# Kernel tuning notes

Hardware: AMD Instinct MI355X
Metric: run time of the kernel (lower is better)

The kernel has to match this reference:

```python
import jax, jax.numpy as jnp
import numpy as np
from jax import lax

B, N, C, NP, NS, H, L = 2, 16384, 256, 2048, 32, 4, 2
DFF = 2 * C
RADIUS = 1.0
EPS = 1e-5


def setup_inputs() -> dict:
    key = jax.random.key(0)
    ks = jax.random.split(key, 12)
    s = 0.02
    f32 = jnp.float32
    return {
        "xyz": jax.random.normal(ks[0], (B, N, 3), f32),
        "features": jax.random.normal(ks[1], (B, C, N), f32),
        # positional encoding: Conv1x1(3->C/2)+BN(eval)+ReLU, Conv1x1(C/2->C)
        "pe1_w": jax.random.normal(ks[2], (C // 2, 3), f32) * s,
        "pe1_b": jnp.zeros((C // 2,), f32),
        "bn_g": jnp.ones((C // 2,), f32),
        "bn_b": jnp.zeros((C // 2,), f32),
        "bn_m": jnp.zeros((C // 2,), f32),
        "bn_v": jnp.ones((C // 2,), f32),
        "pe2_w": jax.random.normal(ks[3], (C, C // 2), f32) * s,
        "pe2_b": jnp.zeros((C,), f32),
        # L pre-norm transformer encoder layers (stacked on leading dim)
        "ipw": jax.random.normal(ks[4], (L, 3 * C, C), f32) * s,
        "ipb": jnp.zeros((L, 3 * C), f32),
        "opw": jax.random.normal(ks[5], (L, C, C), f32) * s,
        "opb": jnp.zeros((L, C), f32),
        "ln1s": jnp.ones((L, C), f32), "ln1b": jnp.zeros((L, C), f32),
        "ln2s": jnp.ones((L, C), f32), "ln2b": jnp.zeros((L, C), f32),
        "fc1w": jax.random.normal(ks[6], (L, DFF, C), f32) * s,
        "fc1b": jnp.zeros((L, DFF), f32),
        "fc2w": jax.random.normal(ks[7], (L, C, DFF), f32) * s,
        "fc2b": jnp.zeros((L, C), f32),
    }


def _fps(xyz, npoint):
    # D-FPS starting from point 0 (pointnet2 convention). xyz: [B,N,3]
    b, n, _ = xyz.shape

    def step(carry, _):
        dists, far = carry
        centroid = jnp.take_along_axis(xyz, far[:, None, None], axis=1)  # [B,1,3]
        d = jnp.sum((xyz - centroid) ** 2, -1)
        dists = jnp.minimum(dists, d)
        return (dists, jnp.argmax(dists, -1).astype(jnp.int32)), far

    init = (jnp.full((b, n), 1e10, jnp.float32), jnp.zeros((b,), jnp.int32))
    _, idx = lax.scan(step, init, None, length=npoint)
    return idx.T  # [B, npoint]


def _ball_query(xyz, new_xyz, radius, ns):
    # first <=ns points within radius, padded with the first hit. [B,NP,NS]
    n = xyz.shape[1]
    d2 = jnp.sum((new_xyz[:, :, None, :] - xyz[:, None, :, :]) ** 2, -1)  # [B,NP,N]
    scores = jnp.where(d2 < radius * radius, jnp.arange(n, dtype=jnp.int32), n)
    svals = jnp.sort(scores, axis=-1)[..., :ns]
    order = jnp.argsort(scores, axis=-1)[..., :ns].astype(jnp.int32)
    valid = svals < n
    return jnp.where(valid, order, order[..., :1])


def _ln(x, s, b):
    m = jnp.mean(x, -1, keepdims=True)
    v = jnp.var(x, -1, keepdims=True)
    return (x - m) * lax.rsqrt(v + EPS) * s + b


def _mha(x, w, bias, ow, ob):
    # x: [S, Bn, D] (seq-first, like nn.MultiheadAttention)
    S, Bn, D = x.shape
    hd = D // H
    qkv = x @ w.T + bias
    q, k, v = jnp.split(qkv, 3, -1)
    rs = lambda t: t.reshape(S, Bn, H, hd).transpose(1, 2, 0, 3)  # [Bn,H,S,hd]
    q, k, v = rs(q), rs(k), rs(v)
    att = jax.nn.softmax(jnp.einsum('bhqd,bhkd->bhqk', q, k) * (1.0 / np.sqrt(hd)), -1)
    o = jnp.einsum('bhqk,bhkd->bhqd', att, v).transpose(2, 0, 1, 3).reshape(S, Bn, D)
    return o @ ow.T + ob


def reference(xyz, features, pe1_w, pe1_b, bn_g, bn_b, bn_m, bn_v, pe2_w, pe2_b,
              ipw, ipb, opw, opb, ln1s, ln1b, ln2s, ln2b, fc1w, fc1b, fc2w, fc2b):
    # --- sample + group ---
    fps_idx = _fps(lax.stop_gradient(xyz), NP)                       # [B,NP]
    new_xyz = jnp.take_along_axis(xyz, fps_idx[:, :, None], axis=1)  # [B,NP,3]
    idx = _ball_query(lax.stop_gradient(xyz), lax.stop_gradient(new_xyz), RADIUS, NS)
    g_xyz = jax.vmap(lambda p, i: p[i])(xyz, idx) - new_xyz[:, :, None, :]  # [B,NP,NS,3]
    g_xyz = g_xyz.transpose(0, 3, 1, 2)                              # [B,3,NP,NS]
    g_feat = jax.vmap(lambda f, i: f[:, i])(features, idx)           # [B,C,NP,NS]
    # --- positional encoding (conv1x1 + BN(eval) + ReLU, conv1x1) ---
    h = jnp.einsum('oc,bcps->bops', pe1_w, g_xyz) + pe1_b[None, :, None, None]
    h = (h - bn_m[None, :, None, None]) * lax.rsqrt(bn_v + EPS)[None, :, None, None]
    h = jax.nn.relu(h * bn_g[None, :, None, None] + bn_b[None, :, None, None])
    pe = jnp.einsum('oc,bcps->bops', pe2_w, h) + pe2_b[None, :, None, None]
    x = g_feat + pe                                                  # [B,C,NP,NS]
    # --- local transformer over each neighborhood (seq len = NS) ---
    x = x.transpose(0, 2, 1, 3).reshape(B * NP, C, NS).transpose(2, 0, 1)  # [NS,B*NP,C]
    for l in range(L):
        x = _ln(x, ln1s[l], ln1b[l])
        x = x + _mha(x, ipw[l], ipb[l], opw[l], opb[l])
        x = _ln(x, ln2s[l], ln2b[l])
        x = x + jax.nn.relu(x @ fc1w[l].T + fc1b[l]) @ fc2w[l].T + fc2b[l]
    tf = x.transpose(1, 2, 0).reshape(B, NP, C, NS).transpose(0, 2, 1, 3)  # [B,C,NP,NS]
    Lf = NP * NS

    def scat(feat_b, tf_b, idx_b):
        idx_f = idx_b.reshape(-1)          # [Lf]
        ff = tf_b.reshape(C, -1)           # [C,Lf]
        pos = jnp.arange(Lf, dtype=jnp.int32)
        first = jax.ops.segment_min(pos, idx_f, num_segments=N)  # [N], maxint if absent
        valid = first < Lf
        safe = jnp.where(valid, first, 0)
        return jnp.where(valid[None, :], ff[:, safe], feat_b)    # [C,N]

    out = jax.vmap(scat)(features, tf, idx)  # [B,C,N]
    return out.transpose(0, 2, 1)            # [B,N,C]
```

## Files before the change

kernel.cpp:

```cpp
#include <hip/hip_runtime.h>

#define NB 2
#define NN 16384
#define NC 256
#define NPp 2048
#define NSs 32
#define NH 4
#define HDh 64
#define NL 2
#define NDFF 512
#define LFv (NPp*NSs)
#define LNEPS 1e-5f
#define NBLK 256
#define NTHR 512

typedef short s16x8 __attribute__((ext_vector_type(8)));
typedef float f32x4 __attribute__((ext_vector_type(4)));
typedef float f32x2 __attribute__((ext_vector_type(2)));
typedef unsigned short u16;
typedef unsigned long long u64;

struct CtlBlock { int prog[2]; int ctr1; int ctr2; int bar; };

__device__ __forceinline__ u16 f2bf(float f){
  unsigned u = __float_as_uint(f);
  u += 0x7fffu + ((u>>16)&1u);
  return (u16)(u>>16);
}

__device__ __forceinline__ f32x4 mfma16(s16x8 a, s16x8 b, f32x4 c){
  return __builtin_amdgcn_mfma_f32_16x16x32_bf16(a, b, c, 0, 0, 0);
}

__device__ __forceinline__ f32x2 pk_add(f32x2 a, f32x2 b){
  f32x2 d; asm("v_pk_add_f32 %0, %1, %2" : "=v"(d) : "v"(a), "v"(b)); return d;
}
__device__ __forceinline__ f32x2 pk_mul(f32x2 a, f32x2 b){
  f32x2 d; asm("v_pk_mul_f32 %0, %1, %2" : "=v"(d) : "v"(a), "v"(b)); return d;
}

#define DPP_FMAX(v, ctrl) do { \
  int _iv = __float_as_int(v); \
  int _sh = __builtin_amdgcn_update_dpp(_iv, _iv, (ctrl), 0xF, 0xF, false); \
  (v) = fmaxf((v), __int_as_float(_sh)); \
} while(0)

#define DPP_IMIN(v, ctrl) do { \
  int _sh = __builtin_amdgcn_update_dpp((v), (v), (ctrl), 0xF, 0xF, false); \
  (v) = (_sh < (v)) ? _sh : (v); \
} while(0)

struct SMem {
  u64  masks[256];
  u64  keybuf[4];
  float xs[32][NC];
  u16  xn[32][264];
  u16  qb[32][776];
  u16  pb[NH][32][40];
  int  idx_sh[32];
  float gx_sh[32][3];
  float wcoord[2][8][4];
  int  misc[16];
  int  win[32];
};

__global__ void k_prep(const float* __restrict__ ipw, const float* __restrict__ opw,
                       const float* __restrict__ fc1w, const float* __restrict__ fc2w,
                       const float* __restrict__ pe2w,
                       const float* __restrict__ bng, const float* __restrict__ bnb,
                       const float* __restrict__ bnm, const float* __restrict__ bnv,
                       u16* ipwb, u16* opwb, u16* fc1wb, u16* fc2wb, u16* pe2wb,
                       float* bnsc, float* bnsh, int* first, CtlBlock* ctl){
  const int i0 = blockIdx.x*blockDim.x + threadIdx.x;
  const int stride = gridDim.x*blockDim.x;
  for (int i=i0; i<NL*768*NC; i+=stride) ipwb[i] = f2bf(ipw[i]);
  for (int i=i0; i<NL*NC*NC; i+=stride)  opwb[i] = f2bf(opw[i]);
  for (int i=i0; i<NL*NDFF*NC; i+=stride) fc1wb[i] = f2bf(fc1w[i]);
  for (int i=i0; i<NL*NC*NDFF; i+=stride) fc2wb[i] = f2bf(fc2w[i]);
  for (int i=i0; i<NC*128; i+=stride)    pe2wb[i] = f2bf(pe2w[i]);
  for (int i=i0; i<NB*NN; i+=stride)     first[i] = LFv;
  for (int i=i0; i<128; i+=stride){
    float sc = bng[i]*rsqrtf(bnv[i]+LNEPS);
    bnsc[i] = sc; bnsh[i] = bnb[i] - bnm[i]*sc;
  }
  if (i0 == 0){
    ctl->prog[0] = -1; ctl->prog[1] = -1;
    ctl->ctr1 = 0; ctl->ctr2 = 0; ctl->bar = 0;
  }
}

__global__ __launch_bounds__(256) void k_featT(const float* __restrict__ feat,
                                               float* __restrict__ featT){
  __shared__ float T[32][33];
  const int b = blockIdx.y;
  const int n0 = blockIdx.x*32;
  const int t = threadIdx.x;
  const int tn = t & 31, tc = t >> 5;
  for (int cb=0; cb<NC; cb+=32){
    #pragma unroll
    for (int i=0;i<32;i+=8)
      T[tc+i][tn] = feat[((size_t)b*NC + cb+tc+i)*NN + n0+tn];
    __syncthreads();
    #pragma unroll
    for (int i=0;i<32;i+=8)
      featT[((size_t)b*NN + n0+tc+i)*NC + cb+tn] = T[tn][tc+i];
    __syncthreads();
  }
}

__device__ void fps_run(int b, const float* __restrict__ xyz,
                        float* __restrict__ newxyz, CtlBlock* ctl, SMem& sm){
#pragma clang fp contract(off)
  const int t = threadIdx.x;
  const int lane = t & 63, wid = t >> 6;
  const float* xb = xyz + (size_t)b*NN*3;
  f32x2 px2[16], py2[16], pz2[16], dd2[16];
  #pragma unroll
  for (int m=0;m<16;m++){
    int i0 = t + (2*m)*NTHR, i1 = t + (2*m+1)*NTHR;
    px2[m] = f32x2{xb[i0*3],   xb[i1*3]};
    py2[m] = f32x2{xb[i0*3+1], xb[i1*3+1]};
    pz2[m] = f32x2{xb[i0*3+2], xb[i1*3+2]};
    dd2[m] = f32x2{1e10f, 1e10f};
  }
  if (t < 4) sm.keybuf[t] = 0ull;
  float wx = xb[0], wy = xb[1], wz = xb[2];
  if (t==0){
    newxyz[(size_t)b*NPp*3+0]=wx;
    newxyz[(size_t)b*NPp*3+1]=wy;
    newxyz[(size_t)b*NPp*3+2]=wz;
    __hip_atomic_store(&ctl->prog[b], 0, __ATOMIC_RELEASE, __HIP_MEMORY_SCOPE_AGENT);
  }
  float ncx=-wx, ncy=-wy, ncz=-wz;
  __syncthreads();
  for (int step=1; step<NPp; ++step){
    const f32x2 ncx2={ncx,ncx}, ncy2={ncy,ncy}, ncz2={ncz,ncz};
    #pragma unroll
    for (int m=0;m<16;m++){
      f32x2 dx = pk_add(px2[m], ncx2);
      f32x2 dy = pk_add(py2[m], ncy2);
      f32x2 dz = pk_add(pz2[m], ncz2);
      f32x2 s  = pk_add(pk_add(pk_mul(dx,dx), pk_mul(dy,dy)), pk_mul(dz,dz));
      f32x2 d  = dd2[m];
      d.x = fminf(d.x, s.x);
      d.y = fminf(d.y, s.y);
      dd2[m] = d;
    }
    float h8[8];
    #pragma unroll
    for (int q=0;q<8;q++)
      h8[q] = fmaxf(fmaxf(dd2[2*q].x, dd2[2*q].y), fmaxf(dd2[2*q+1].x, dd2[2*q+1].y));
    float M = fmaxf(fmaxf(fmaxf(h8[0],h8[1]),fmaxf(h8[2],h8[3])),
                    fmaxf(fmaxf(h8[4],h8[5]),fmaxf(h8[6],h8[7])));
    DPP_FMAX(M, 0x111); DPP_FMAX(M, 0x112); DPP_FMAX(M, 0x114); DPP_FMAX(M, 0x118);
    DPP_FMAX(M, 0x142); DPP_FMAX(M, 0x143);
    const unsigned Mb = (unsigned)__builtin_amdgcn_readlane(__float_as_int(M), 63);
    const float Ms = __int_as_float((int)Mb);
    int li = 0x7fffffff;
    #pragma unroll
    for (int m=15;m>=0;m--){
      if (dd2[m].y == Ms) li = t + (2*m+1)*NTHR;
      if (dd2[m].x == Ms) li = t + (2*m)*NTHR;
    }
    DPP_IMIN(li, 0x111); DPP_IMIN(li, 0x112); DPP_IMIN(li, 0x114); DPP_IMIN(li, 0x118);
    DPP_IMIN(li, 0x142); DPP_IMIN(li, 0x143);
    const int li63 = __builtin_amdgcn_readlane(li, 63);
    const int kb = step & 3, cb = step & 1;
    if (lane==0){
      u64 key = ((u64)Mb << 32) | (unsigned)(0x7fffffff - li63);
      atomicMax(&sm.keybuf[kb], key);
      const float* cp = xb + (size_t)li63*3;
      sm.wcoord[cb][wid][0]=cp[0]; sm.wcoord[cb][wid][1]=cp[1]; sm.wcoord[cb][wid][2]=cp[2];
    }
    __syncthreads();
    const u64 kk = sm.keybuf[kb];
    const int widx = 0x7fffffff - (int)(unsigned)(kk & 0xffffffffu);
    const int wv = (widx & (NTHR-1)) >> 6;
    const float nx = sm.wcoord[cb][wv][0];
    const float ny = sm.wcoord[cb][wv][1];
    const float nz = sm.wcoord[cb][wv][2];
    ncx=-nx; ncy=-ny; ncz=-nz;
    if (t==0){
      newxyz[((size_t)b*NPp+step)*3+0]=nx;
      newxyz[((size_t)b*NPp+step)*3+1]=ny;
      newxyz[((size_t)b*NPp+step)*3+2]=nz;
      sm.keybuf[(step+2)&3] = 0ull;
      if ((step & 7) == 7 || step == NPp-1)
        __hip_atomic_store(&ctl->prog[b], step, __ATOMIC_RELEASE, __HIP_MEMORY_SCOPE_AGENT);
    }
  }
}

__device__ void seq_ballq(const float* __restrict__ xb, float cx, float cy, float cz,
                          SMem& sm, int t, int lane, int wid){
#pragma clang fp contract(off)
  for (int it=0; it<32; ++it){
    int cid = wid*32 + it;
    int i = cid*64 + lane;
    float dx=xb[i*3]-cx, dy=xb[i*3+1]-cy, dz=xb[i*3+2]-cz;
    float d2=(dx*dx+dy*dy)+dz*dz;
    u64 m = __ballot(d2 < 1.0f);
    if (lane==0) sm.masks[cid] = m;
  }
  __syncthreads();
  if (wid==0){
    u64 mk[4]; int cnt=0;
    #pragma unroll
    for (int j=0;j<4;j++){ mk[j]=sm.masks[lane*4+j]; cnt += __popcll(mk[j]); }
    int inc = cnt;
    #pragma unroll
    for (int ofs=1; ofs<64; ofs<<=1){
      int v = __shfl_up(inc, ofs);
      if (lane >= ofs) inc += v;
    }
    int r = inc - cnt;
    int tot = __shfl(inc, 63);
    #pragma unroll
    for (int j=0;j<4;j++){
      u64 msk = mk[j];
      int base = (lane*4+j)*64;
      while (msk && r < NSs){
        int bpos = __ffsll(msk)-1;
        sm.idx_sh[r] = base + bpos;
        msk &= msk-1;
        ++r;
      }
      if (r >= NSs) break;
    }
    int cc = tot < NSs ? tot : NSs;
    int pv = (tot > 0) ? sm.idx_sh[0] : 0;
    if (lane < NSs && lane >= cc) sm.idx_sh[lane] = pv;
  }
  __syncthreads();
}

__device__ __forceinline__ void ln_block512(SMem& sm, const float* __restrict__ s_,
                                            const float* __restrict__ b_, int t){
  const int s = t >> 4, j = t & 15;
  float v[16];
  float sum = 0.f;
  #pragma unroll
  for (int k=0;k<16;k++){ v[k]=sm.xs[s][j*16+k]; sum += v[k]; }
  #pragma unroll
  for (int m=1;m<16;m<<=1) sum += __shfl_xor(sum, m);
  const float mean = sum * (1.f/256.f);
  float vs = 0.f;
  #pragma unroll
  for (int k=0;k<16;k++){ float d=v[k]-mean; vs += d*d; }
  #pragma unroll
  for (int m=1;m<16;m<<=1) vs += __shfl_xor(vs, m);
  const float rstd = rsqrtf(vs*(1.f/256.f) + LNEPS);
  #pragma unroll
  for (int k=0;k<16;k++){
    int c = j*16+k;
    float y = (v[k]-mean)*rstd*s_[c] + b_[c];
    sm.xs[s][c] = y;
    sm.xn[s][c] = f2bf(y);
  }
}

__device__ void seq_pe_tf(SMem& sm, int b, int p,
    const float* __restrict__ xyz, const float* __restrict__ features,
    const float* __restrict__ featT, int useT, const float* __restrict__ newxyz,
    const float* __restrict__ pe1w, const float* __restrict__ pe1b,
    const float* __restrict__ bnsc, const float* __restrict__ bnsh,
    const u16* __restrict__ pe2wb, const float* __restrict__ pe2b,
    const u16* __restrict__ ipwb, const float* __restrict__ ipb,
    const u16* __restrict__ opwb, const float* __restrict__ opb,
    const float* __restrict__ ln1s, const float* __restrict__ ln1b,
    const float* __restrict__ ln2s, const float* __restrict__ ln2b,
    const u16* __restrict__ fc1wb, const float* __restrict__ fc1b,
    const u16* __restrict__ fc2wb, const float* __restrict__ fc2b){
  const int t = threadIdx.x, lane = t & 63, wid = t >> 6;
  const int c15 = lane & 15, g4 = lane >> 4;

  if (t < 96){
    int s = t/3, d = t%3;
    sm.gx_sh[s][d] = xyz[((size_t)b*NN + sm.idx_sh[s])*3 + d] - newxyz[(size_t)p*3 + d];
  }
  if (useT){
    for (int e=t; e<32*NC; e+=NTHR){
      int s=e>>8, c=e&255;
      sm.xs[s][c] = featT[((size_t)b*NN + sm.idx_sh[s])*NC + c];
    }
  } else {
    for (int e=t; e<32*NC; e+=NTHR){
      int s=e>>8, c=e&255;
      sm.xs[s][c] = features[((size_t)b*NC + c)*NN + sm.idx_sh[s]];
    }
  }
  __syncthreads();
  for (int i=t; i<32*128; i+=NTHR){
    int s = i >> 7, o = i & 127;
    float h = pe1w[o*3]*sm.gx_sh[s][0] + pe1w[o*3+1]*sm.gx_sh[s][1] + pe1w[o*3+2]*sm.gx_sh[s][2] + pe1b[o];
    h = h*bnsc[o] + bnsh[o];
    sm.xn[s][o] = f2bf(h > 0.f ? h : 0.f);
  }
  __syncthreads();
  for (int tt=wid; tt<32; tt+=8){
    int m0 = (tt & 1)*16, n0 = (tt >> 1)*16;
    f32x4 acc = {0.f,0.f,0.f,0.f};
    #pragma unroll
    for (int kk=0; kk<4; kk++){
      s16x8 a = *(const s16x8*)&sm.xn[m0+c15][kk*32 + g4*8];
      s16x8 bb = *(const s16x8*)&pe2wb[(size_t)(n0+c15)*128 + kk*32 + g4*8];
      acc = mfma16(a, bb, acc);
    }
    int col = n0 + c15;
    float bias = pe2b[col];
    #pragma unroll
    for (int r=0;r<4;r++) sm.xs[m0 + g4*4 + r][col] += acc[r] + bias;
  }
  __syncthreads();

  for (int l=0; l<NL; ++l){
    ln_block512(sm, ln1s + l*NC, ln1b + l*NC, t);
    __syncthreads();
    const u16* Wq = ipwb + (size_t)l*768*NC;
    const float* bq = ipb + l*768;
    for (int tt=wid; tt<96; tt+=8){
      int m0 = (tt & 1)*16, n0 = (tt >> 1)*16;
      f32x4 acc = {0.f,0.f,0.f,0.f};
      #pragma unroll
      for (int kk=0;kk<8;kk++){
        s16x8 a = *(const s16x8*)&sm.xn[m0+c15][kk*32 + g4*8];
        s16x8 bb = *(const s16x8*)&Wq[(size_t)(n0+c15)*NC + kk*32 + g4*8];
        acc = mfma16(a, bb, acc);
      }
      int col = n0 + c15;
      float bias = bq[col];
      #pragma unroll
      for (int r=0;r<4;r++) sm.qb[m0 + g4*4 + r][col] = f2bf(acc[r] + bias);
    }
    __syncthreads();
    {
      const int h = wid & 3;
      const int mt = wid >> 2;
      f32x4 lac[2];
      #pragma unroll
      for (int nt=0;nt<2;nt++){
        f32x4 acc = {0.f,0.f,0.f,0.f};
        #pragma unroll
        for (int kk=0;kk<2;kk++){
          s16x8 a = *(const s16x8*)&sm.qb[mt*16+c15][h*HDh + kk*32 + g4*8];
          s16x8 bb = *(const s16x8*)&sm.qb[nt*16+c15][256 + h*HDh + kk*32 + g4*8];
          acc = mfma16(a, bb, acc);
        }
        lac[nt] = acc;
      }
      #pragma unroll
      for (int r=0;r<4;r++){
        float v0 = lac[0][r]*0.125f, v1 = lac[1][r]*0.125f;
        float mx = fmaxf(v0, v1);
        #pragma unroll
        for (int m=1;m<16;m<<=1) mx = fmaxf(mx, __shfl_xor(mx, m));
        float e0 = expf(v0-mx), e1 = expf(v1-mx);
        float smm = e0 + e1;
        #pragma unroll
        for (int m=1;m<16;m<<=1) smm += __shfl_xor(smm, m);
        float inv = 1.f/smm;
        int row = mt*16 + g4*4 + r;
        sm.pb[h][row][c15]    = f2bf(e0*inv);
        sm.pb[h][row][16+c15] = f2bf(e1*inv);
      }
      f32x4 oac[4];
      #pragma unroll
      for (int nt=0;nt<4;nt++){
        s16x8 bb;
        #pragma unroll
        for (int e=0;e<8;e++) bb[e] = (short)sm.qb[g4*8+e][512 + h*HDh + nt*16 + c15];
        f32x4 acc = {0.f,0.f,0.f,0.f};
        s16x8 a = *(const s16x8*)&sm.pb[h][mt*16+c15][g4*8];
        oac[nt] = mfma16(a, bb, acc);
      }
      __syncthreads();
      #pragma unroll
      for (int nt=0;nt<4;nt++)
        #pragma unroll
        for (int r=0;r<4;r++)
          sm.xn[mt*16 + g4*4 + r][h*HDh + nt*16 + c15] = f2bf(oac[nt][r]);
    }
    __syncthreads();
    const u16* Wo = opwb + (size_t)l*NC*NC;
    const float* bo = opb + l*NC;
    for (int tt=wid; tt<32; tt+=8){
      int m0 = (tt & 1)*16, n0 = (tt >> 1)*16;
      f32x4 acc = {0.f,0.f,0.f,0.f};
      #pragma unroll
      for (int kk=0;kk<8;kk++){
        s16x8 a = *(const s16x8*)&sm.xn[m0+c15][kk*32 + g4*8];
        s16x8 bb = *(const s16x8*)&Wo[(size_t)(n0+c15)*NC + kk*32 + g4*8];
        acc = mfma16(a, bb, acc);
      }
      int col = n0 + c15;
      float bias = bo[col];
      #pragma unroll
      for (int r=0;r<4;r++) sm.xs[m0 + g4*4 + r][col] += acc[r] + bias;
    }
    __syncthreads();
    ln_block512(sm, ln2s + l*NC, ln2b + l*NC, t);
    __syncthreads();
    const u16* W1 = fc1wb + (size_t)l*NDFF*NC;
    for (int tt=wid; tt<64; tt+=8){
      int m0 = (tt & 1)*16, n0 = (tt >> 1)*16;
      f32x4 acc = {0.f,0.f,0.f,0.f};
      #pragma unroll
      for (int kk=0;kk<8;kk++){
        s16x8 a = *(const s16x8*)&sm.xn[m0+c15][kk*32 + g4*8];
        s16x8 bb = *(const s16x8*)&W1[(size_t)(n0+c15)*NC + kk*32 + g4*8];
        acc = mfma16(a, bb, acc);
      }
      int col = n0 + c15;
      float bias = fc1b[l*NDFF + col];
      #pragma unroll
      for (int r=0;r<4;r++){
        float v = acc[r] + bias;
        sm.qb[m0 + g4*4 + r][col] = f2bf(v > 0.f ? v : 0.f);
      }
    }
    __syncthreads();
    const u16* W2 = fc2wb + (size_t)l*NC*NDFF;
    for (int tt=wid; tt<32; tt+=8){
      int m0 = (tt & 1)*16, n0 = (tt >> 1)*16;
      f32x4 acc = {0.f,0.f,0.f,0.f};
      #pragma unroll
      for (int kk=0;kk<16;kk++){
        s16x8 a = *(const s16x8*)&sm.qb[m0+c15][kk*32 + g4*8];
        s16x8 bb = *(const s16x8*)&W2[(size_t)(n0+c15)*NDFF + kk*32 + g4*8];
        acc = mfma16(a, bb, acc);
      }
      int col = n0 + c15;
      float bias = fc2b[l*NC + col];
      #pragma unroll
      for (int r=0;r<4;r++) sm.xs[m0 + g4*4 + r][col] += acc[r] + bias;
    }
    __syncthreads();
  }
}

__global__ __launch_bounds__(NTHR,1) void k_mega(
    const float* __restrict__ xyz, const float* __restrict__ features,
    const float* __restrict__ featT, int useT,
    float* __restrict__ newxyz, int* __restrict__ first, CtlBlock* ctl,
    const float* __restrict__ pe1w, const float* __restrict__ pe1b,
    const float* __restrict__ bnsc, const float* __restrict__ bnsh,
    const u16* __restrict__ pe2wb, const float* __restrict__ pe2b,
    const u16* __restrict__ ipwb, const float* __restrict__ ipb,
    const u16* __restrict__ opwb, const float* __restrict__ opb,
    const float* __restrict__ ln1s, const float* __restrict__ ln1b,
    const float* __restrict__ ln2s, const float* __restrict__ ln2b,
    const u16* __restrict__ fc1wb, const float* __restrict__ fc1b,
    const u16* __restrict__ fc2wb, const float* __restrict__ fc2b,
    float* __restrict__ out){
  __shared__ SMem sm;
  const int t = threadIdx.x, lane = t & 63, wid = t >> 6;

  if (blockIdx.x < NB){
    fps_run(blockIdx.x, xyz, newxyz, ctl, sm);
  } else {
    for (;;){
      if (t==0) sm.misc[1] = atomicAdd(&ctl->ctr1, 1);
      __syncthreads();
      int p = sm.misc[1];
      if (p >= NB*NPp) break;
      int b = p >> 11, pp = p & (NPp-1);
      if (t==0){
        while (__hip_atomic_load(&ctl->prog[b], __ATOMIC_RELAXED, __HIP_MEMORY_SCOPE_AGENT) < pp)
          __builtin_amdgcn_s_sleep(2);
        __builtin_amdgcn_fence(__ATOMIC_ACQUIRE, "agent");
      }
      __syncthreads();
      float cx = newxyz[(size_t)p*3], cy = newxyz[(size_t)p*3+1], cz = newxyz[(size_t)p*3+2];
      seq_ballq(xyz + (size_t)b*NN*3, cx, cy, cz, sm, t, lane, wid);
      if (t < NSs) atomicMin(&first[b*NN + sm.idx_sh[t]], pp*NSs + t);
      __syncthreads();
    }
  }

  __syncthreads();
  if (t==0){
    __builtin_amdgcn_fence(__ATOMIC_RELEASE, "agent");
    __hip_atomic_fetch_add(&ctl->bar, 1, __ATOMIC_RELAXED, __HIP_MEMORY_SCOPE_AGENT);
    while (__hip_atomic_load(&ctl->bar, __ATOMIC_RELAXED, __HIP_MEMORY_SCOPE_AGENT) < NBLK)
      __builtin_amdgcn_s_sleep(8);
    __builtin_amdgcn_fence(__ATOMIC_ACQUIRE, "agent");
  }
  __syncthreads();

  for (;;){
    if (t==0) sm.misc[1] = atomicAdd(&ctl->ctr2, 1);
    __syncthreads();
    int p = sm.misc[1];
    if (p >= NB*NPp) break;
    int b = p >> 11, pp = p & (NPp-1);
    float cx = newxyz[(size_t)p*3], cy = newxyz[(size_t)p*3+1], cz = newxyz[(size_t)p*3+2];
    seq_ballq(xyz + (size_t)b*NN*3, cx, cy, cz, sm, t, lane, wid);
    if (t==0) sm.misc[2] = 0;
    __syncthreads();
    if (t < NSs){
      int pos = pp*NSs + t;
      int f = __hip_atomic_load(&first[b*NN + sm.idx_sh[t]], __ATOMIC_RELAXED, __HIP_MEMORY_SCOPE_AGENT);
      int w = (f == pos) ? 1 : 0;
      sm.win[t] = w;
      if (w) atomicOr(&sm.misc[2], 1);
    }
    __syncthreads();
    if (!sm.misc[2]) continue;
    seq_pe_tf(sm, b, p, xyz, features, featT, useT, newxyz,
              pe1w, pe1b, bnsc, bnsh, pe2wb, pe2b, ipwb, ipb, opwb, opb,
              ln1s, ln1b, ln2s, ln2b, fc1wb, fc1b, fc2wb, fc2b);
    for (int e=t; e<NSs*NC; e+=NTHR){
      int s = e >> 8, c = e & 255;
      if (sm.win[s]) out[((size_t)b*NN + sm.idx_sh[s])*NC + c] = sm.xs[s][c];
    }
    __syncthreads();
  }
}

__global__ __launch_bounds__(256) void k_outfill_T(const float* __restrict__ featT,
                                                   const int* __restrict__ first,
                                                   float* __restrict__ out){
  const int t = threadIdx.x;
  for (int rr=0; rr<8; ++rr){
    int row = blockIdx.x*8 + rr;
    if (first[row] == LFv)
      out[(size_t)row*NC + t] = featT[(size_t)row*NC + t];
  }
}

__global__ __launch_bounds__(256) void k_outfill_noT(const float* __restrict__ feat,
                                                     const int* __restrict__ first,
                                                     float* __restrict__ out){
  __shared__ float T[32][33];
  const int b = blockIdx.y;
  const int n0 = blockIdx.x*32;
  const int t = threadIdx.x;
  const int tn = t & 31, tc = t >> 5;
  for (int cb=0; cb<NC; cb+=32){
    #pragma unroll
    for (int i=0;i<32;i+=8)
      T[tc+i][tn] = feat[((size_t)b*NC + cb+tc+i)*NN + n0+tn];
    __syncthreads();
    #pragma unroll
    for (int i=0;i<32;i+=8){
      int n = n0 + tc + i;
      if (first[b*NN+n] == LFv)
        out[((size_t)b*NN + n)*NC + cb+tn] = T[tn][tc+i];
    }
    __syncthreads();
  }
}

extern "C" void kernel_launch(void* const* d_in, const int* in_sizes, int n_in,
                              void* d_out, int out_size, void* d_ws, size_t ws_size,
                              hipStream_t stream){
  const float* xyz   = (const float*)d_in[0];
  const float* feat  = (const float*)d_in[1];
  const float* pe1w  = (const float*)d_in[2];
  const float* pe1b  = (const float*)d_in[3];
  const float* bng   = (const float*)d_in[4];
  const float* bnb   = (const float*)d_in[5];
  const float* bnm   = (const float*)d_in[6];
  const float* bnv   = (const float*)d_in[7];
  const float* pe2w  = (const float*)d_in[8];
  const float* pe2b  = (const float*)d_in[9];
  const float* ipw   = (const float*)d_in[10];
  const float* ipb   = (const float*)d_in[11];
  const float* opw   = (const float*)d_in[12];
  const float* opb   = (const float*)d_in[13];
  const float* ln1s  = (const float*)d_in[14];
  const float* ln1b  = (const float*)d_in[15];
  const float* ln2s  = (const float*)d_in[16];
  const float* ln2b  = (const float*)d_in[17];
  const float* fc1w  = (const float*)d_in[18];
  const float* fc1b  = (const float*)d_in[19];
  const float* fc2w  = (const float*)d_in[20];
  const float* fc2b  = (const float*)d_in[21];
  float* out = (float*)d_out;

  char* ws = (char*)d_ws;
  size_t off = 0;
  auto alloc = [&](size_t bytes)->void*{
    void* p = ws + off;
    off = (off + bytes + 255) & ~(size_t)255;
    return p;
  };
  float* newxyz  = (float*)alloc((size_t)NB*NPp*3*4);
  int*   first   = (int*)  alloc((size_t)NB*NN*4);
  CtlBlock* ctl  = (CtlBlock*)alloc(sizeof(CtlBlock));
  float* bnsc    = (float*)alloc(128*4);
  float* bnsh    = (float*)alloc(128*4);
  u16*   ipwb    = (u16*)  alloc((size_t)NL*768*NC*2);
  u16*   opwb    = (u16*)  alloc((size_t)NL*NC*NC*2);
  u16*   fc1wb   = (u16*)  alloc((size_t)NL*NDFF*NC*2);
  u16*   fc2wb   = (u16*)  alloc((size_t)NL*NC*NDFF*2);
  u16*   pe2wb   = (u16*)  alloc((size_t)NC*128*2);
  float* featT   = (float*)(ws + off);
  int useT = (off + (size_t)NB*NN*NC*4 <= ws_size) ? 1 : 0;

  k_prep<<<512, 256, 0, stream>>>(ipw, opw, fc1w, fc2w, pe2w, bng, bnb, bnm, bnv,
                                  ipwb, opwb, fc1wb, fc2wb, pe2wb, bnsc, bnsh, first, ctl);
  if (useT)
    k_featT<<<dim3(NN/32, NB), 256, 0, stream>>>(feat, featT);

  const float* featT_c = featT;
  void* kargs[] = {
    (void*)&xyz, (void*)&feat, (void*)&featT_c, (void*)&useT,
    (void*)&newxyz, (void*)&first, (void*)&ctl,
    (void*)&pe1w, (void*)&pe1b, (void*)&bnsc, (void*)&bnsh,
    (void*)&pe2wb, (void*)&pe2b, (void*)&ipwb, (void*)&ipb,
    (void*)&opwb, (void*)&opb, (void*)&ln1s, (void*)&ln1b,
    (void*)&ln2s, (void*)&ln2b, (void*)&fc1wb, (void*)&fc1b,
    (void*)&fc2wb, (void*)&fc2b, (void*)&out };
  hipLaunchCooperativeKernel((void*)k_mega, dim3(NBLK), dim3(NTHR), kargs, 0, stream);

  if (useT)
    k_outfill_T<<<(NB*NN)/8, 256, 0, stream>>>(featT, first, out);
  else
    k_outfill_noT<<<dim3(NN/32, NB), 256, 0, stream>>>(feat, first, out);
  (void)in_sizes; (void)n_in; (void)out_size;
}
```

Baseline: 4.474 ms.

## Replace FPS progress counter with per-centroid ready flags and register-held winner coords

FPS now takes the winning centroid's coordinates from registers through a slot switch, so it no longer reloads them from global memory. Centroids are batched in shared memory and published every 8 steps as packed u64 stores, each followed by a per-point ready flag. Consumers spin on their own point's flag instead of a shared progress counter. Launch bounds change to allow 2 blocks per CU, the xs row is padded, and the max reduction is fused into the distance loop. The risks are ordering, since the flags are relaxed stores after a manual waitcnt with no acquire fence, and added register pressure from the switch.

After: 4.693 ms. 4.9% more time.

```diff
diff --git a/kernel.cpp b/kernel.cpp
--- a/kernel.cpp
+++ b/kernel.cpp
@@ -13,6 +13,7 @@
 #define LNEPS 1e-5f
 #define NBLK 256
 #define NTHR 512
+#define NW 8
 
 typedef short s16x8 __attribute__((ext_vector_type(8)));
 typedef float f32x4 __attribute__((ext_vector_type(4)));
@@ -20,7 +21,7 @@
 typedef unsigned short u16;
 typedef unsigned long long u64;
 
-struct CtlBlock { int prog[2]; int ctr1; int ctr2; int bar; };
+struct CtlBlock { int ctr1; int ctr2; int bar; };
 
 __device__ __forceinline__ u16 f2bf(float f){
   unsigned u = __float_as_uint(f);
@@ -53,13 +54,14 @@
 struct SMem {
   u64  masks[256];
   u64  keybuf[4];
-  float xs[32][NC];
+  float wvc[2][NW][4];
+  float cxbuf[8][4];
+  float xs[32][260];
   u16  xn[32][264];
   u16  qb[32][776];
   u16  pb[NH][32][40];
   int  idx_sh[32];
   float gx_sh[32][3];
-  float wcoord[2][8][4];
   int  misc[16];
   int  win[32];
 };
@@ -70,7 +72,7 @@
                        const float* __restrict__ bng, const float* __restrict__ bnb,
                        const float* __restrict__ bnm, const float* __restrict__ bnv,
                        u16* ipwb, u16* opwb, u16* fc1wb, u16* fc2wb, u16* pe2wb,
-                       float* bnsc, float* bnsh, int* first, CtlBlock* ctl){
+                       float* bnsc, float* bnsh, int* first, int* rdy, CtlBlock* ctl){
   const int i0 = blockIdx.x*blockDim.x + threadIdx.x;
   const int stride = gridDim.x*blockDim.x;
   for (int i=i0; i<NL*768*NC; i+=stride) ipwb[i] = f2bf(ipw[i]);
@@ -79,14 +81,12 @@
   for (int i=i0; i<NL*NC*NDFF; i+=stride) fc2wb[i] = f2bf(fc2w[i]);
   for (int i=i0; i<NC*128; i+=stride)    pe2wb[i] = f2bf(pe2w[i]);
   for (int i=i0; i<NB*NN; i+=stride)     first[i] = LFv;
+  for (int i=i0; i<NB*NPp; i+=stride)    rdy[i] = 0;
   for (int i=i0; i<128; i+=stride){
     float sc = bng[i]*rsqrtf(bnv[i]+LNEPS);
     bnsc[i] = sc; bnsh[i] = bnb[i] - bnm[i]*sc;
   }
-  if (i0 == 0){
-    ctl->prog[0] = -1; ctl->prog[1] = -1;
-    ctl->ctr1 = 0; ctl->ctr2 = 0; ctl->bar = 0;
-  }
+  if (i0 == 0){ ctl->ctr1 = 0; ctl->ctr2 = 0; ctl->bar = 0; }
 }
 
 __global__ __launch_bounds__(256) void k_featT(const float* __restrict__ feat,
@@ -108,8 +108,10 @@
   }
 }
 
-__device__ void fps_run(int b, const float* __restrict__ xyz,
-                        float* __restrict__ newxyz, CtlBlock* ctl, SMem& sm){
+#define SELC(S) case S: scx = px2[(S)>>1][(S)&1]; scy = py2[(S)>>1][(S)&1]; scz = pz2[(S)>>1][(S)&1]; break;
+
+__device__ void fps_run(int b, const float* __restrict__ xyz, u64* __restrict__ cx2,
+                        int* __restrict__ rdy, SMem& sm){
 #pragma clang fp contract(off)
   const int t = threadIdx.x;
   const int lane = t & 63, wid = t >> 6;
@@ -124,38 +126,31 @@
     dd2[m] = f32x2{1e10f, 1e10f};
   }
   if (t < 4) sm.keybuf[t] = 0ull;
-  float wx = xb[0], wy = xb[1], wz = xb[2];
-  if (t==0){
-    newxyz[(size_t)b*NPp*3+0]=wx;
-    newxyz[(size_t)b*NPp*3+1]=wy;
-    newxyz[(size_t)b*NPp*3+2]=wz;
-    __hip_atomic_store(&ctl->prog[b], 0, __ATOMIC_RELEASE, __HIP_MEMORY_SCOPE_AGENT);
-  }
-  float ncx=-wx, ncy=-wy, ncz=-wz;
+  float ncx, ncy, ncz;
+  {
+    float wx = xb[0], wy = xb[1], wz = xb[2];
+    ncx=-wx; ncy=-wy; ncz=-wz;
+    if (t==0){ sm.cxbuf[0][0]=wx; sm.cxbuf[0][1]=wy; sm.cxbuf[0][2]=wz; }
+  }
   __syncthreads();
   for (int step=1; step<NPp; ++step){
     const f32x2 ncx2={ncx,ncx}, ncy2={ncy,ncy}, ncz2={ncz,ncz};
+    float bestv = -1.f;
     #pragma unroll
     for (int m=0;m<16;m++){
       f32x2 dx = pk_add(px2[m], ncx2);
       f32x2 dy = pk_add(py2[m], ncy2);
       f32x2 dz = pk_add(pz2[m], ncz2);
       f32x2 s  = pk_add(pk_add(pk_mul(dx,dx), pk_mul(dy,dy)), pk_mul(dz,dz));
-      f32x2 d  = dd2[m];
-      d.x = fminf(d.x, s.x);
-      d.y = fminf(d.y, s.y);
-      dd2[m] = d;
-    }
-    float h8[8];
-    #pragma unroll
-    for (int q=0;q<8;q++)
-      h8[q] = fmaxf(fmaxf(dd2[2*q].x, dd2[2*q].y), fmaxf(dd2[2*q+1].x, dd2[2*q+1].y));
-    float M = fmaxf(fmaxf(fmaxf(h8[0],h8[1]),fmaxf(h8[2],h8[3])),
-                    fmaxf(fmaxf(h8[4],h8[5]),fmaxf(h8[6],h8[7])));
+      dd2[m].x = fminf(dd2[m].x, s.x);
+      dd2[m].y = fminf(dd2[m].y, s.y);
+      bestv = fmaxf(fmaxf(bestv, dd2[m].x), dd2[m].y);
+    }
+    float M = bestv;
     DPP_FMAX(M, 0x111); DPP_FMAX(M, 0x112); DPP_FMAX(M, 0x114); DPP_FMAX(M, 0x118);
     DPP_FMAX(M, 0x142); DPP_FMAX(M, 0x143);
-    const unsigned Mb = (unsigned)__builtin_amdgcn_readlane(__float_as_int(M), 63);
-    const float Ms = __int_as_float((int)Mb);
+    const int Mi = __builtin_amdgcn_readlane(__float_as_int(M), 63);
+    const float Ms = __int_as_float(Mi);
     int li = 0x7fffffff;
     #pragma unroll
     for (int m=15;m>=0;m--){
@@ -167,26 +162,50 @@
     const int li63 = __builtin_amdgcn_readlane(li, 63);
     const int kb = step & 3, cb = step & 1;
     if (lane==0){
-      u64 key = ((u64)Mb << 32) | (unsigned)(0x7fffffff - li63);
+      u64 key = ((u64)(unsigned)Mi << 32) | (unsigned)(0x7fffffff - li63);
       atomicMax(&sm.keybuf[kb], key);
-      const float* cp = xb + (size_t)li63*3;
-      sm.wcoord[cb][wid][0]=cp[0]; sm.wcoord[cb][wid][1]=cp[1]; sm.wcoord[cb][wid][2]=cp[2];
+    }
+    {
+      const int slot = li63 >> 9;
+      float scx=0.f, scy=0.f, scz=0.f;
+      switch(slot){
+        SELC(0) SELC(1) SELC(2) SELC(3) SELC(4) SELC(5) SELC(6) SELC(7)
+        SELC(8) SELC(9) SELC(10) SELC(11) SELC(12) SELC(13) SELC(14) SELC(15)
+        SELC(16) SELC(17) SELC(18) SELC(19) SELC(20) SELC(21) SELC(22) SELC(23)
+        SELC(24) SELC(25) SELC(26) SELC(27) SELC(28) SELC(29) SELC(30) SELC(31)
+        default: break;
+      }
+      if (t == (li63 & (NTHR-1))){
+        sm.wvc[cb][wid][0]=scx; sm.wvc[cb][wid][1]=scy; sm.wvc[cb][wid][2]=scz;
+      }
     }
     __syncthreads();
     const u64 kk = sm.keybuf[kb];
-    const int widx = 0x7fffffff - (int)(unsigned)(kk & 0xffffffffu);
+    const int widx = 0x7fffffff - (int)(unsigned)(kk & 0xffffffffull);
     const int wv = (widx & (NTHR-1)) >> 6;
-    const float nx = sm.wcoord[cb][wv][0];
-    const float ny = sm.wcoord[cb][wv][1];
-    const float nz = sm.wcoord[cb][wv][2];
-    ncx=-nx; ncy=-ny; ncz=-nz;
+    const float bx = sm.wvc[cb][wv][0];
+    const float by = sm.wvc[cb][wv][1];
+    const float bz = sm.wvc[cb][wv][2];
+    ncx=-bx; ncy=-by; ncz=-bz;
     if (t==0){
-      newxyz[((size_t)b*NPp+step)*3+0]=nx;
-      newxyz[((size_t)b*NPp+step)*3+1]=ny;
-      newxyz[((size_t)b*NPp+step)*3+2]=nz;
-      sm.keybuf[(step+2)&3] = 0ull;
-      if ((step & 7) == 7 || step == NPp-1)
-        __hip_atomic_store(&ctl->prog[b], step, __ATOMIC_RELEASE, __HIP_MEMORY_SCOPE_AGENT);
+      sm.cxbuf[step & 7][0]=bx; sm.cxbuf[step & 7][1]=by; sm.cxbuf[step & 7][2]=bz;
+      sm.keybuf[(step+2) & 3] = 0ull;
+      if ((step & 7) == 7){
+        int s0 = step - 7;
+        #pragma unroll
+        for (int j=0;j<8;j++){
+          float fx=sm.cxbuf[j][0], fy=sm.cxbuf[j][1], fz=sm.cxbuf[j][2];
+          u64 lo = ((u64)__float_as_uint(fy) << 32) | __float_as_uint(fx);
+          u64 hi = (u64)__float_as_uint(fz);
+          size_t pb2 = (size_t)(b*NPp + s0 + j)*2;
+          __hip_atomic_store(&cx2[pb2],   lo, __ATOMIC_RELAXED, __HIP_MEMORY_SCOPE_AGENT);
+          __hip_atomic_store(&cx2[pb2+1], hi, __ATOMIC_RELAXED, __HIP_MEMORY_SCOPE_AGENT);
+        }
+        asm volatile("s_waitcnt vmcnt(0)" ::: "memory");
+        #pragma unroll
+        for (int j=0;j<8;j++)
+          __hip_atomic_store(&rdy[b*NPp + s0 + j], 1, __ATOMIC_RELAXED, __HIP_MEMORY_SCOPE_AGENT);
+      }
     }
   }
 }
@@ -259,9 +278,9 @@
   }
 }
 
-__device__ void seq_pe_tf(SMem& sm, int b, int p,
+__device__ void seq_pe_tf(SMem& sm, int b, float ccx, float ccy, float ccz,
     const float* __restrict__ xyz, const float* __restrict__ features,
-    const float* __restrict__ featT, int useT, const float* __restrict__ newxyz,
+    const float* __restrict__ featT, int useT,
     const float* __restrict__ pe1w, const float* __restrict__ pe1b,
     const float* __restrict__ bnsc, const float* __restrict__ bnsh,
     const u16* __restrict__ pe2wb, const float* __restrict__ pe2b,
@@ -276,7 +295,8 @@
 
   if (t < 96){
     int s = t/3, d = t%3;
-    sm.gx_sh[s][d] = xyz[((size_t)b*NN + sm.idx_sh[s])*3 + d] - newxyz[(size_t)p*3 + d];
+    float cd = (d==0) ? ccx : ((d==1) ? ccy : ccz);
+    sm.gx_sh[s][d] = xyz[((size_t)b*NN + sm.idx_sh[s])*3 + d] - cd;
   }
   if (useT){
     for (int e=t; e<32*NC; e+=NTHR){
@@ -297,7 +317,7 @@
     sm.xn[s][o] = f2bf(h > 0.f ? h : 0.f);
   }
   __syncthreads();
-  for (int tt=wid; tt<32; tt+=8){
+  for (int tt=wid; tt<32; tt+=NW){
     int m0 = (tt & 1)*16, n0 = (tt >> 1)*16;
     f32x4 acc = {0.f,0.f,0.f,0.f};
     #pragma unroll
@@ -318,7 +338,7 @@
     __syncthreads();
     const u16* Wq = ipwb + (size_t)l*768*NC;
     const float* bq = ipb + l*768;
-    for (int tt=wid; tt<96; tt+=8){
+    for (int tt=wid; tt<96; tt+=NW){
       int m0 = (tt & 1)*16, n0 = (tt >> 1)*16;
       f32x4 acc = {0.f,0.f,0.f,0.f};
       #pragma unroll
@@ -383,7 +403,7 @@
     __syncthreads();
     const u16* Wo = opwb + (size_t)l*NC*NC;
     const float* bo = opb + l*NC;
-    for (int tt=wid; tt<32; tt+=8){
+    for (int tt=wid; tt<32; tt+=NW){
       int m0 = (tt & 1)*16, n0 = (tt >> 1)*16;
       f32x4 acc = {0.f,0.f,0.f,0.f};
       #pragma unroll
@@ -401,7 +421,7 @@
     ln_block512(sm, ln2s + l*NC, ln2b + l*NC, t);
     __syncthreads();
     const u16* W1 = fc1wb + (size_t)l*NDFF*NC;
-    for (int tt=wid; tt<64; tt+=8){
+    for (int tt=wid; tt<64; tt+=NW){
       int m0 = (tt & 1)*16, n0 = (tt >> 1)*16;
       f32x4 acc = {0.f,0.f,0.f,0.f};
       #pragma unroll
@@ -420,7 +440,7 @@
     }
     __syncthreads();
     const u16* W2 = fc2wb + (size_t)l*NC*NDFF;
-    for (int tt=wid; tt<32; tt+=8){
+    for (int tt=wid; tt<32; tt+=NW){
       int m0 = (tt & 1)*16, n0 = (tt >> 1)*16;
       f32x4 acc = {0.f,0.f,0.f,0.f};
       #pragma unroll
@@ -438,10 +458,10 @@
   }
 }
 
-__global__ __launch_bounds__(NTHR,1) void k_mega(
+__global__ __launch_bounds__(NTHR, 2) void k_mega(
     const float* __restrict__ xyz, const float* __restrict__ features,
     const float* __restrict__ featT, int useT,
-    float* __restrict__ newxyz, int* __restrict__ first, CtlBlock* ctl,
+    u64* __restrict__ cx2, int* __restrict__ rdy, int* __restrict__ first, CtlBlock* ctl,
     const float* __restrict__ pe1w, const float* __restrict__ pe1b,
     const float* __restrict__ bnsc, const float* __restrict__ bnsh,
     const u16* __restrict__ pe2wb, const float* __restrict__ pe2b,
@@ -456,7 +476,7 @@
   const int t = threadIdx.x, lane = t & 63, wid = t >> 6;
 
   if (blockIdx.x < NB){
-    fps_run(blockIdx.x, xyz, newxyz, ctl, sm);
+    fps_run(blockIdx.x, xyz, cx2, rdy, sm);
   } else {
     for (;;){
       if (t==0) sm.misc[1] = atomicAdd(&ctl->ctr1, 1);
@@ -465,12 +485,19 @@
       if (p >= NB*NPp) break;
       int b = p >> 11, pp = p & (NPp-1);
       if (t==0){
-        while (__hip_atomic_load(&ctl->prog[b], __ATOMIC_RELAXED, __HIP_MEMORY_SCOPE_AGENT) < pp)
-          __builtin_amdgcn_s_sleep(2);
-        __builtin_amdgcn_fence(__ATOMIC_ACQUIRE, "agent");
+        while (!__hip_atomic_load(&rdy[p], __ATOMIC_RELAXED, __HIP_MEMORY_SCOPE_AGENT))
+          __builtin_amdgcn_s_sleep(16);
+        asm volatile("" ::: "memory");
+        u64 lo = __hip_atomic_load(&cx2[(size_t)p*2],   __ATOMIC_RELAXED, __HIP_MEMORY_SCOPE_AGENT);
+        u64 hi = __hip_atomic_load(&cx2[(size_t)p*2+1], __ATOMIC_RELAXED, __HIP_MEMORY_SCOPE_AGENT);
+        sm.misc[4] = (int)(unsigned)(lo & 0xffffffffull);
+        sm.misc[5] = (int)(unsigned)(lo >> 32);
+        sm.misc[6] = (int)(unsigned)(hi & 0xffffffffull);
       }
       __syncthreads();
-      float cx = newxyz[(size_t)p*3], cy = newxyz[(size_t)p*3+1], cz = newxyz[(size_t)p*3+2];
+      float cx = __int_as_float(sm.misc[4]);
+      float cy = __int_as_float(sm.misc[5]);
+      float cz = __int_as_float(sm.misc[6]);
       seq_ballq(xyz + (size_t)b*NN*3, cx, cy, cz, sm, t, lane, wid);
       if (t < NSs) atomicMin(&first[b*NN + sm.idx_sh[t]], pp*NSs + t);
       __syncthreads();
@@ -493,20 +520,23 @@
     int p = sm.misc[1];
     if (p >= NB*NPp) break;
     int b = p >> 11, pp = p & (NPp-1);
-    float cx = newxyz[(size_t)p*3], cy = newxyz[(size_t)p*3+1], cz = newxyz[(size_t)p*3+2];
+    u64 lo = cx2[(size_t)p*2], hi = cx2[(size_t)p*2+1];
+    float cx = __int_as_float((int)(unsigned)(lo & 0xffffffffull));
+    float cy = __int_as_float((int)(unsigned)(lo >> 32));
+    float cz = __int_as_float((int)(unsigned)(hi & 0xffffffffull));
     seq_ballq(xyz + (size_t)b*NN*3, cx, cy, cz, sm, t, lane, wid);
     if (t==0) sm.misc[2] = 0;
     __syncthreads();
     if (t < NSs){
       int pos = pp*NSs + t;
-      int f = __hip_atomic_load(&first[b*NN + sm.idx_sh[t]], __ATOMIC_RELAXED, __HIP_MEMORY_SCOPE_AGENT);
+      int f = first[b*NN + sm.idx_sh[t]];
       int w = (f == pos) ? 1 : 0;
       sm.win[t] = w;
       if (w) atomicOr(&sm.misc[2], 1);
     }
     __syncthreads();
     if (!sm.misc[2]) continue;
-    seq_pe_tf(sm, b, p, xyz, features, featT, useT, newxyz,
+    seq_pe_tf(sm, b, cx, cy, cz, xyz, features, featT, useT,
               pe1w, pe1b, bnsc, bnsh, pe2wb, pe2b, ipwb, ipb, opwb, opb,
               ln1s, ln1b, ln2s, ln2b, fc1wb, fc1b, fc2wb, fc2b);
     for (int e=t; e<NSs*NC; e+=NTHR){
@@ -585,7 +615,8 @@
     off = (off + bytes + 255) & ~(size_t)255;
     return p;
   };
-  float* newxyz  = (float*)alloc((size_t)NB*NPp*3*4);
+  u64*   cx2     = (u64*)  alloc((size_t)NB*NPp*2*8);
+  int*   rdy     = (int*)  alloc((size_t)NB*NPp*4);
   int*   first   = (int*)  alloc((size_t)NB*NN*4);
   CtlBlock* ctl  = (CtlBlock*)alloc(sizeof(CtlBlock));
   float* bnsc    = (float*)alloc(128*4);
@@ -595,18 +626,19 @@
   u16*   fc1wb   = (u16*)  alloc((size_t)NL*NDFF*NC*2);
   u16*   fc2wb   = (u16*)  alloc((size_t)NL*NC*NDFF*2);
   u16*   pe2wb   = (u16*)  alloc((size_t)NC*128*2);
-  float* featT   = (float*)(ws + off);
   int useT = (off + (size_t)NB*NN*NC*4 <= ws_size) ? 1 : 0;
+  float* featT = (float*)(useT ? alloc((size_t)NB*NN*NC*4) : (void*)ws);
 
   k_prep<<<512, 256, 0, stream>>>(ipw, opw, fc1w, fc2w, pe2w, bng, bnb, bnm, bnv,
-                                  ipwb, opwb, fc1wb, fc2wb, pe2wb, bnsc, bnsh, first, ctl);
+                                  ipwb, opwb, fc1wb, fc2wb, pe2wb, bnsc, bnsh,
+                                  first, rdy, ctl);
   if (useT)
     k_featT<<<dim3(NN/32, NB), 256, 0, stream>>>(feat, featT);
 
   const float* featT_c = featT;
   void* kargs[] = {
     (void*)&xyz, (void*)&feat, (void*)&featT_c, (void*)&useT,
-    (void*)&newxyz, (void*)&first, (void*)&ctl,
+    (void*)&cx2, (void*)&rdy, (void*)&first, (void*)&ctl,
     (void*)&pe1w, (void*)&pe1b, (void*)&bnsc, (void*)&bnsh,
     (void*)&pe2wb, (void*)&pe2b, (void*)&ipwb, (void*)&ipb,
     (void*)&opwb, (void*)&opb, (void*)&ln1s, (void*)&ln1b,
```
